# Optimization experiments

Hardware: AMD Instinct MI355X
Metric: run time of the kernel (lower is better)

## Reference

```python
import jax, jax.numpy as jnp
import numpy as np

VOXEL_SIZE = np.array([0.32, 0.32, 6.0], dtype=np.float32)
SPATIAL_SIZE = np.array([-74.88, 74.88, -74.88, 74.88, -3.0, 3.0], dtype=np.float32)
# voxel_spatial_size = ceil((max-min)/voxel_size) per dim -> [468, 468, 1]
GRID = np.array([int(np.ceil((SPATIAL_SIZE[2*i+1]-SPATIAL_SIZE[2*i])/VOXEL_SIZE[i])) for i in range(3)], dtype=np.int32)
# voxel origin = floor(min / voxel_size) -> [-234, -234, -1]
ORIGIN = np.floor(SPATIAL_SIZE[0::2] / VOXEL_SIZE).astype(np.int32)
VOL = int(np.prod(GRID))  # 468*468*1
# row-major id multipliers: prods[1:]+[1] -> [468, 1, 1]
SHIFT = np.array([int(np.prod(GRID[1:])), int(np.prod(GRID[2:])), 1], dtype=np.int32)
VOXEL_FEATURE_MIN = -1000.0

B, N, D_IN, MLP = 4, 100000, 16, 128


def setup_inputs() -> dict:
    key = jax.random.key(0)
    k1, k2, k3, k4, k5 = jax.random.split(key, 5)
    xy = jax.random.uniform(k1, (B, N, 2), minval=-80.0, maxval=80.0)
    z = jax.random.uniform(k2, (B, N, 1), minval=-4.0, maxval=4.0)
    point_xyz = jnp.concatenate([xy, z], axis=-1)
    point_feature = jax.random.normal(k3, (B, N, D_IN), dtype=jnp.float32)
    point_mask = jax.random.uniform(k4, (B, N)) < 0.95
    W = jax.random.normal(k5, (D_IN + 3, MLP), dtype=jnp.float32) * 0.1
    b = jnp.zeros((MLP,), dtype=jnp.float32)
    return {"point_xyz": point_xyz, "point_feature": point_feature,
            "point_mask": point_mask, "W": W, "b": b}


def reference(point_xyz, point_feature, point_mask, W, b):
    vs = jnp.asarray(VOXEL_SIZE, dtype=point_xyz.dtype)
    # PointToVoxel
    pvx_f = jnp.floor(point_xyz / vs)                      # [B,N,3] float voxel coords
    point_voxel_feature = point_xyz - pvx_f * vs           # delta within voxel
    pvx = pvx_f.astype(jnp.int32) - jnp.asarray(ORIGIN)    # shifted int voxel coords
    grid = jnp.asarray(GRID)
    in_bounds = jnp.all((pvx >= 0) & (pvx < grid), axis=-1)
    voxel_mask = in_bounds & point_mask                    # [B,N]
    vid = jnp.sum(pvx * jnp.asarray(SHIFT), axis=-1)       # [B,N]
    vid = vid + jnp.arange(B, dtype=jnp.int32)[:, None] * VOL
    vid = vid * voxel_mask.astype(jnp.int32)               # invalid -> 0
    # point net (Dense + ReLU) on [point_feature, voxel delta]
    feat = jnp.concatenate([point_feature, point_voxel_feature], axis=-1)
    mf = voxel_mask.astype(feat.dtype)[..., None]
    feat = feat * mf
    feat = jax.nn.relu(jnp.einsum('bnd,dk->bnk', feat, W) + b)
    feat = feat * mf
    # scatter-max into dense voxel grid
    seg = jax.ops.segment_max(feat.reshape(-1, MLP), vid.reshape(-1),
                              num_segments=B * VOL)
    seg = jnp.where(seg > VOXEL_FEATURE_MIN, seg, 0.0)
    # z dim is 1 -> squeezed: [B, 468, 468, MLP]
    return seg.reshape(B, int(GRID[0]), int(GRID[1]), MLP)
```

## Files before the change

kernel.cpp:

```cpp
#include <hip/hip_runtime.h>
#include <hip/hip_bf16.h>
#include <stdint.h>

#define BB   4
#define NN   100000
#define DIN  16
#define DF   19
#define KO   128
#define GX   468
#define GY   468
#define VOL  (GX * GY)
#define TOTAL (BB * NN)

__global__ __launch_bounds__(256) void zero_fill(float4* __restrict__ out, int n4) {
    int i = blockIdx.x * 256 + threadIdx.x;
    const int stride = gridDim.x * 256;
    const float4 z = make_float4(0.f, 0.f, 0.f, 0.f);
    for (; i < n4; i += stride) out[i] = z;
}

__global__ void detect_mask_kind(const uint4* __restrict__ mask_words,
                                 int* __restrict__ flag) {
    __shared__ int sA, sB;
    if (threadIdx.x == 0) { sA = 0; sB = 0; }
    __syncthreads();
    int a = 0, b = 0;
    #pragma unroll
    for (int it = 0; it < 4; ++it) {
        uint4 w = mask_words[it * 256 + threadIdx.x];
        unsigned lo = (w.x & 0xFFu) | (w.y & 0xFFu) | (w.z & 0xFFu) | (w.w & 0xFFu);
        unsigned hi = (w.x & 0xFFFFFF00u) | (w.y & 0xFFFFFF00u) |
                      (w.z & 0xFFFFFF00u) | (w.w & 0xFFFFFF00u);
        if (hi) a = 1;
        if (lo) b = 1;
    }
    if (a) atomicOr(&sA, 1);
    if (b) atomicOr(&sB, 1);
    __syncthreads();
    if (threadIdx.x == 0) flag[0] = (sA && sB) ? 1 : 4;
}

__global__ __launch_bounds__(256) void voxelize_kernel(
    const float* __restrict__ xyz,
    const float* __restrict__ pfeat,
    const unsigned char* __restrict__ mask_raw,
    const float* __restrict__ W,
    const float* __restrict__ bias,
    const int*   __restrict__ flag,
    float* __restrict__ out)
{
    __shared__ float sW[DF * KO];
    __shared__ float sb[KO];
    for (int i = threadIdx.x; i < DF * KO; i += 256) sW[i] = W[i];
    if (threadIdx.x < KO) sb[threadIdx.x] = bias[threadIdx.x];
    __syncthreads();

    const int elem4 = (flag[0] == 4);
    const int lane  = threadIdx.x & 63;
    const int wave  = blockIdx.x * 4 + (threadIdx.x >> 6);
    const int nwaves = gridDim.x * 4;
    const int chunk = (TOTAL + nwaves - 1) / nwaves;
    const int p0 = wave * chunk;
    const int p1 = min(p0 + chunk, TOTAL);

    const float b0 = sb[lane];
    const float b1 = sb[lane + 64];

    for (int p = p0; p < p1; ++p) {
        const float x = xyz[p * 3 + 0];
        const float y = xyz[p * 3 + 1];
        const float z = xyz[p * 3 + 2];
        bool m;
        if (elem4) m = (((const int*)mask_raw)[p] != 0);
        else       m = (mask_raw[p] != 0);
        const float fx = floorf(x / 0.32f);
        const float fy = floorf(y / 0.32f);
        const float fz = floorf(z / 6.0f);
        const int ix = (int)fx + 234;
        const int iy = (int)fy + 234;
        const int iz = (int)fz + 1;
        const bool inb = ((unsigned)ix < (unsigned)GX) &
                         ((unsigned)iy < (unsigned)GY) &
                         (iz == 0) & m;
        if (!inb) continue;

        float f[DF];
        const float4* pf4 = (const float4*)(pfeat + (size_t)p * DIN);
        float4 v0 = pf4[0], v1 = pf4[1], v2 = pf4[2], v3 = pf4[3];
        f[0]=v0.x; f[1]=v0.y; f[2]=v0.z; f[3]=v0.w;
        f[4]=v1.x; f[5]=v1.y; f[6]=v1.z; f[7]=v1.w;
        f[8]=v2.x; f[9]=v2.y; f[10]=v2.z; f[11]=v2.w;
        f[12]=v3.x; f[13]=v3.y; f[14]=v3.z; f[15]=v3.w;
        f[16] = x - fx * 0.32f;
        f[17] = y - fy * 0.32f;
        f[18] = z - fz * 6.0f;

        float acc0 = b0, acc1 = b1;
        #pragma unroll
        for (int d = 0; d < DF; ++d) {
            acc0 = fmaf(f[d], sW[d * KO + lane], acc0);
            acc1 = fmaf(f[d], sW[d * KO + 64 + lane], acc1);
        }
        acc0 = fmaxf(acc0, 0.0f);
        acc1 = fmaxf(acc1, 0.0f);

        const int bidx = p / NN;
        float* dst = out + (size_t)(bidx * VOL + ix * GY + iy) * KO;
        if (acc0 > 0.0f)
            atomicMax((int*)(dst + lane), __float_as_int(acc0));
        if (acc1 > 0.0f)
            atomicMax((int*)(dst + lane + 64), __float_as_int(acc1));
    }
}

extern "C" void kernel_launch(void* const* d_in, const int* in_sizes, int n_in,
                              void* d_out, int out_size, void* d_ws, size_t ws_size,
                              hipStream_t stream) {
    const float* xyz   = (const float*)d_in[0];
    const float* pfeat = (const float*)d_in[1];
    const unsigned char* mask = (const unsigned char*)d_in[2];
    const float* W     = (const float*)d_in[3];
    const float* bias  = (const float*)d_in[4];
    float* out = (float*)d_out;
    int*   flag = (int*)d_ws;

    const int n4 = out_size / 4;
    zero_fill<<<4096, 256, 0, stream>>>((float4*)out, n4);
    detect_mask_kind<<<1, 256, 0, stream>>>((const uint4*)mask, flag);
    voxelize_kernel<<<2048, 256, 0, stream>>>(xyz, pfeat, mask, W, bias, flag, out);
}
```

Baseline: 595.6 us.

## Replace atomic scatter-max with counting sort and per-voxel gather reduction

Points are bucketed by voxel using a count pass, a three-level prefix scan and a scatter into a sorted point list. One wave per voxel then recomputes the dense layer for its points, takes the max in registers and writes the output once, which folds in the separate zero-fill pass. This removes the global float atomicMax traffic and the full-output zero fill, in exchange for several extra small kernels and workspace buffers. Empty voxels are handled by the same kernel that writes the output.

```diff
diff --git a/kernel.cpp b/kernel.cpp
--- a/kernel.cpp
+++ b/kernel.cpp
@@ -4,20 +4,23 @@
 
 #define BB   4
 #define NN   100000
+#define TOTAL (BB * NN)
 #define DIN  16
 #define DF   19
 #define KO   128
 #define GX   468
 #define GY   468
 #define VOL  (GX * GY)
-#define TOTAL (BB * NN)
-
-__global__ __launch_bounds__(256) void zero_fill(float4* __restrict__ out, int n4) {
-    int i = blockIdx.x * 256 + threadIdx.x;
-    const int stride = gridDim.x * 256;
-    const float4 z = make_float4(0.f, 0.f, 0.f, 0.f);
-    for (; i < n4; i += stride) out[i] = z;
-}
+#define NV   (BB * VOL)
+#define NBLK ((NV + 1023) / 1024)
+
+#define WS_COUNTS   0
+#define WS_OFFSETS  (NV)
+#define WS_BSUM     (2 * NV)
+#define WS_PVID     (2 * NV + 1024)
+#define WS_PRANK    (2 * NV + 1024 + TOTAL)
+#define WS_PLIST    (2 * NV + 1024 + 2 * TOTAL)
+#define WS_FLAG     (2 * NV + 1024 + 3 * TOTAL)
 
 __global__ void detect_mask_kind(const uint4* __restrict__ mask_words,
                                  int* __restrict__ flag) {
@@ -40,50 +43,143 @@
     if (threadIdx.x == 0) flag[0] = (sA && sB) ? 1 : 4;
 }
 
-__global__ __launch_bounds__(256) void voxelize_kernel(
+__global__ __launch_bounds__(256) void zero_counts(int4* __restrict__ counts4) {
+    int i = blockIdx.x * 256 + threadIdx.x;
+    if (i < NV / 4) counts4[i] = make_int4(0, 0, 0, 0);
+}
+
+__global__ __launch_bounds__(256) void pass1_count(
+    const float* __restrict__ xyz,
+    const unsigned char* __restrict__ mask_raw,
+    const int* __restrict__ flag,
+    int* __restrict__ counts,
+    int* __restrict__ pvid,
+    int* __restrict__ prank)
+{
+    const int p = blockIdx.x * 256 + threadIdx.x;
+    if (p >= TOTAL) return;
+    const float x = xyz[p * 3 + 0];
+    const float y = xyz[p * 3 + 1];
+    const float z = xyz[p * 3 + 2];
+    bool m;
+    if (flag[0] == 4) m = (((const int*)mask_raw)[p] != 0);
+    else              m = (mask_raw[p] != 0);
+    const int ix = (int)floorf(x / 0.32f) + 234;
+    const int iy = (int)floorf(y / 0.32f) + 234;
+    const int iz = (int)floorf(z / 6.0f) + 1;
+    const bool inb = ((unsigned)ix < (unsigned)GX) &
+                     ((unsigned)iy < (unsigned)GY) &
+                     (iz == 0) & m;
+    int vid = -1;
+    if (inb) {
+        vid = (p / NN) * VOL + ix * GY + iy;
+        prank[p] = atomicAdd(&counts[vid], 1);
+    }
+    pvid[p] = vid;
+}
+
+__global__ __launch_bounds__(256) void scan_bsum(const int* __restrict__ counts,
+                                                 int* __restrict__ bsum) {
+    __shared__ int sdata[256];
+    const int t = threadIdx.x;
+    const int base = blockIdx.x * 1024 + t * 4;
+    int s = 0;
+    #pragma unroll
+    for (int j = 0; j < 4; ++j) {
+        const int i = base + j;
+        if (i < NV) s += counts[i];
+    }
+    sdata[t] = s;
+    __syncthreads();
+    for (int off = 128; off > 0; off >>= 1) {
+        if (t < off) sdata[t] += sdata[t + off];
+        __syncthreads();
+    }
+    if (t == 0) bsum[blockIdx.x] = sdata[0];
+}
+
+__global__ __launch_bounds__(1024) void scan_top(int* __restrict__ bsum) {
+    __shared__ int s[1024];
+    const int t = threadIdx.x;
+    const int v = (t < NBLK) ? bsum[t] : 0;
+    s[t] = v;
+    __syncthreads();
+    for (int off = 1; off < 1024; off <<= 1) {
+        const int tmp = (t >= off) ? s[t - off] : 0;
+        __syncthreads();
+        s[t] += tmp;
+        __syncthreads();
+    }
+    if (t < NBLK) bsum[t] = s[t] - v;
+}
+
+__global__ __launch_bounds__(256) void scan_offsets(const int* __restrict__ counts,
+                                                    const int* __restrict__ bsum,
+                                                    int* __restrict__ offsets) {
+    __shared__ int sdata[256];
+    const int t = threadIdx.x;
+    const int i0 = blockIdx.x * 1024 + t * 4;
+    int c[4];
+    #pragma unroll
+    for (int j = 0; j < 4; ++j)
+        c[j] = (i0 + j < NV) ? counts[i0 + j] : 0;
+    const int tsum = c[0] + c[1] + c[2] + c[3];
+    sdata[t] = tsum;
+    __syncthreads();
+    for (int off = 1; off < 256; off <<= 1) {
+        const int tmp = (t >= off) ? sdata[t - off] : 0;
+        __syncthreads();
+        sdata[t] += tmp;
+        __syncthreads();
+    }
+    int excl = sdata[t] - tsum + bsum[blockIdx.x];
+    #pragma unroll
+    for (int j = 0; j < 4; ++j) {
+        if (i0 + j < NV) { offsets[i0 + j] = excl; excl += c[j]; }
+    }
+}
+
+__global__ __launch_bounds__(256) void pass2_scatter(
+    const int* __restrict__ pvid,
+    const int* __restrict__ prank,
+    const int* __restrict__ offsets,
+    int* __restrict__ plist)
+{
+    const int p = blockIdx.x * 256 + threadIdx.x;
+    if (p >= TOTAL) return;
+    const int v = pvid[p];
+    if (v >= 0) plist[offsets[v] + prank[p]] = p;
+}
+
+__global__ __launch_bounds__(256) void pass3_write(
     const float* __restrict__ xyz,
     const float* __restrict__ pfeat,
-    const unsigned char* __restrict__ mask_raw,
     const float* __restrict__ W,
     const float* __restrict__ bias,
-    const int*   __restrict__ flag,
+    const int* __restrict__ counts,
+    const int* __restrict__ offsets,
+    const int* __restrict__ plist,
     float* __restrict__ out)
 {
-    __shared__ float sW[DF * KO];
-    __shared__ float sb[KO];
-    for (int i = threadIdx.x; i < DF * KO; i += 256) sW[i] = W[i];
-    if (threadIdx.x < KO) sb[threadIdx.x] = bias[threadIdx.x];
-    __syncthreads();
-
-    const int elem4 = (flag[0] == 4);
-    const int lane  = threadIdx.x & 63;
-    const int wave  = blockIdx.x * 4 + (threadIdx.x >> 6);
-    const int nwaves = gridDim.x * 4;
-    const int chunk = (TOTAL + nwaves - 1) / nwaves;
-    const int p0 = wave * chunk;
-    const int p1 = min(p0 + chunk, TOTAL);
-
-    const float b0 = sb[lane];
-    const float b1 = sb[lane + 64];
-
-    for (int p = p0; p < p1; ++p) {
+    const int lane = threadIdx.x & 63;
+    const int v = blockIdx.x * 4 + (threadIdx.x >> 6);
+    const int c = counts[v];
+    float2* dst = (float2*)(out + (size_t)v * KO) + lane;
+    if (c == 0) { *dst = make_float2(0.f, 0.f); return; }
+
+    const int o = offsets[v];
+    const float2* W2 = (const float2*)W;
+    float2 w[DF];
+    #pragma unroll
+    for (int d = 0; d < DF; ++d) w[d] = W2[d * 64 + lane];
+    const float2 bb = ((const float2*)bias)[lane];
+
+    float m0 = -3.0e38f, m1 = -3.0e38f;
+    for (int j = 0; j < c; ++j) {
+        const int p = plist[o + j];
         const float x = xyz[p * 3 + 0];
         const float y = xyz[p * 3 + 1];
         const float z = xyz[p * 3 + 2];
-        bool m;
-        if (elem4) m = (((const int*)mask_raw)[p] != 0);
-        else       m = (mask_raw[p] != 0);
-        const float fx = floorf(x / 0.32f);
-        const float fy = floorf(y / 0.32f);
-        const float fz = floorf(z / 6.0f);
-        const int ix = (int)fx + 234;
-        const int iy = (int)fy + 234;
-        const int iz = (int)fz + 1;
-        const bool inb = ((unsigned)ix < (unsigned)GX) &
-                         ((unsigned)iy < (unsigned)GY) &
-                         (iz == 0) & m;
-        if (!inb) continue;
-
         float f[DF];
         const float4* pf4 = (const float4*)(pfeat + (size_t)p * DIN);
         float4 v0 = pf4[0], v1 = pf4[1], v2 = pf4[2], v3 = pf4[3];
@@ -91,26 +187,20 @@
         f[4]=v1.x; f[5]=v1.y; f[6]=v1.z; f[7]=v1.w;
         f[8]=v2.x; f[9]=v2.y; f[10]=v2.z; f[11]=v2.w;
         f[12]=v3.x; f[13]=v3.y; f[14]=v3.z; f[15]=v3.w;
-        f[16] = x - fx * 0.32f;
-        f[17] = y - fy * 0.32f;
-        f[18] = z - fz * 6.0f;
-
-        float acc0 = b0, acc1 = b1;
+        f[16] = x - floorf(x / 0.32f) * 0.32f;
+        f[17] = y - floorf(y / 0.32f) * 0.32f;
+        f[18] = z - floorf(z / 6.0f) * 6.0f;
+
+        float a0 = bb.x, a1 = bb.y;
         #pragma unroll
         for (int d = 0; d < DF; ++d) {
-            acc0 = fmaf(f[d], sW[d * KO + lane], acc0);
-            acc1 = fmaf(f[d], sW[d * KO + 64 + lane], acc1);
+            a0 = fmaf(f[d], w[d].x, a0);
+            a1 = fmaf(f[d], w[d].y, a1);
         }
-        acc0 = fmaxf(acc0, 0.0f);
-        acc1 = fmaxf(acc1, 0.0f);
-
-        const int bidx = p / NN;
-        float* dst = out + (size_t)(bidx * VOL + ix * GY + iy) * KO;
-        if (acc0 > 0.0f)
-            atomicMax((int*)(dst + lane), __float_as_int(acc0));
-        if (acc1 > 0.0f)
-            atomicMax((int*)(dst + lane + 64), __float_as_int(acc1));
-    }
+        m0 = fmaxf(m0, a0);
+        m1 = fmaxf(m1, a1);
+    }
+    *dst = make_float2(fmaxf(m0, 0.f), fmaxf(m1, 0.f));
 }
 
 extern "C" void kernel_launch(void* const* d_in, const int* in_sizes, int n_in,
@@ -122,10 +212,25 @@
     const float* W     = (const float*)d_in[3];
     const float* bias  = (const float*)d_in[4];
     float* out = (float*)d_out;
-    int*   flag = (int*)d_ws;
-
-    const int n4 = out_size / 4;
-    zero_fill<<<4096, 256, 0, stream>>>((float4*)out, n4);
+    int* ws = (int*)d_ws;
+
+    int* counts  = ws + WS_COUNTS;
+    int* offsets = ws + WS_OFFSETS;
+    int* bsum    = ws + WS_BSUM;
+    int* pvid    = ws + WS_PVID;
+    int* prank   = ws + WS_PRANK;
+    int* plist   = ws + WS_PLIST;
+    int* flag    = ws + WS_FLAG;
+
     detect_mask_kind<<<1, 256, 0, stream>>>((const uint4*)mask, flag);
-    voxelize_kernel<<<2048, 256, 0, stream>>>(xyz, pfeat, mask, W, bias, flag, out);
-}
+    zero_counts<<<(NV / 4 + 255) / 256, 256, 0, stream>>>((int4*)counts);
+    pass1_count<<<(TOTAL + 255) / 256, 256, 0, stream>>>(xyz, mask, flag,
+                                                         counts, pvid, prank);
+    scan_bsum<<<NBLK, 256, 0, stream>>>(counts, bsum);
+    scan_top<<<1, 1024, 0, stream>>>(bsum);
+    scan_offsets<<<NBLK, 256, 0, stream>>>(counts, bsum, offsets);
+    pass2_scatter<<<(TOTAL + 255) / 256, 256, 0, stream>>>(pvid, prank,
+                                                           offsets, plist);
+    pass3_write<<<NV / 4, 256, 0, stream>>>(xyz, pfeat, W, bias,
+                                            counts, offsets, plist, out);
+}
```

Measured after the change: 654.5 us. +9.9%, slower.

## Bin points per voxel, then gather and reduce max without atomics

Applied to the files above, without the earlier changes.

Replaces the per-point scatter with float atomicMax by a two-pass scheme. The first pass bins point indices into fixed-capacity per-voxel lists using atomic counters. The second pass walks every voxel, recomputes the MLP for its points, takes the max in registers and writes the voxel row with plain stores. It also merges zero-fill and mask detection into one prep kernel. The costs are extra workspace (counts plus a CAP=16 list per voxel), a zeroing pass over the counts, redundant zero-filling of output that gather_write mostly overwrites, and silent truncation if a voxel ever holds more than 16 points.

```diff
diff --git a/kernel.cpp b/kernel.cpp
--- a/kernel.cpp
+++ b/kernel.cpp
@@ -4,112 +4,136 @@
 
 #define BB   4
 #define NN   100000
+#define TOTAL (BB * NN)
 #define DIN  16
 #define DF   19
 #define KO   128
 #define GX   468
 #define GY   468
 #define VOL  (GX * GY)
-#define TOTAL (BB * NN)
+#define NV   (BB * VOL)
+#define CAP  16
 
-__global__ __launch_bounds__(256) void zero_fill(float4* __restrict__ out, int n4) {
-    int i = blockIdx.x * 256 + threadIdx.x;
+#define WS_COUNTS   0
+#define WS_PLIST    (NV)
+#define WS_FLAG     (NV + NV * CAP)
+
+__global__ __launch_bounds__(256) void prep(
+    float4* __restrict__ out4,
+    int4*   __restrict__ counts4,
+    const uint4* __restrict__ mask_words,
+    int* __restrict__ flag)
+{
+    if (blockIdx.x == 0) {
+        __shared__ int sA, sB;
+        if (threadIdx.x == 0) { sA = 0; sB = 0; }
+        __syncthreads();
+        int a = 0, b = 0;
+        #pragma unroll
+        for (int it = 0; it < 4; ++it) {
+            uint4 w = mask_words[it * 256 + threadIdx.x];
+            unsigned lo = (w.x & 0xFFu) | (w.y & 0xFFu) | (w.z & 0xFFu) | (w.w & 0xFFu);
+            unsigned hi = (w.x & 0xFFFFFF00u) | (w.y & 0xFFFFFF00u) |
+                          (w.z & 0xFFFFFF00u) | (w.w & 0xFFFFFF00u);
+            if (hi) a = 1;
+            if (lo) b = 1;
+        }
+        if (a) atomicOr(&sA, 1);
+        if (b) atomicOr(&sB, 1);
+        __syncthreads();
+        if (threadIdx.x == 0) flag[0] = (sA && sB) ? 1 : 4;
+    }
+
     const int stride = gridDim.x * 256;
-    const float4 z = make_float4(0.f, 0.f, 0.f, 0.f);
-    for (; i < n4; i += stride) out[i] = z;
+    const int gid = blockIdx.x * 256 + threadIdx.x;
+    const float4 zf = make_float4(0.f, 0.f, 0.f, 0.f);
+    for (int i = gid; i < NV * (KO / 4); i += stride) out4[i] = zf;
+    const int4 zi = make_int4(0, 0, 0, 0);
+    for (int i = gid; i < NV / 4; i += stride) counts4[i] = zi;
 }
 
-__global__ void detect_mask_kind(const uint4* __restrict__ mask_words,
-                                 int* __restrict__ flag) {
-    __shared__ int sA, sB;
-    if (threadIdx.x == 0) { sA = 0; sB = 0; }
-    __syncthreads();
-    int a = 0, b = 0;
-    #pragma unroll
-    for (int it = 0; it < 4; ++it) {
-        uint4 w = mask_words[it * 256 + threadIdx.x];
-        unsigned lo = (w.x & 0xFFu) | (w.y & 0xFFu) | (w.z & 0xFFu) | (w.w & 0xFFu);
-        unsigned hi = (w.x & 0xFFFFFF00u) | (w.y & 0xFFFFFF00u) |
-                      (w.z & 0xFFFFFF00u) | (w.w & 0xFFFFFF00u);
-        if (hi) a = 1;
-        if (lo) b = 1;
+__global__ __launch_bounds__(256) void pass1_bin(
+    const float* __restrict__ xyz,
+    const unsigned char* __restrict__ mask_raw,
+    const int* __restrict__ flag,
+    int* __restrict__ counts,
+    int* __restrict__ plist)
+{
+    const int p = blockIdx.x * 256 + threadIdx.x;
+    if (p >= TOTAL) return;
+    const float x = xyz[p * 3 + 0];
+    const float y = xyz[p * 3 + 1];
+    const float z = xyz[p * 3 + 2];
+    bool m;
+    if (flag[0] == 4) m = (((const int*)mask_raw)[p] != 0);
+    else              m = (mask_raw[p] != 0);
+    const int ix = (int)floorf(x / 0.32f) + 234;
+    const int iy = (int)floorf(y / 0.32f) + 234;
+    const int iz = (int)floorf(z / 6.0f) + 1;
+    const bool inb = ((unsigned)ix < (unsigned)GX) &
+                     ((unsigned)iy < (unsigned)GY) &
+                     (iz == 0) & m;
+    if (inb) {
+        const int vid = (p / NN) * VOL + ix * GY + iy;
+        const int rank = atomicAdd(&counts[vid], 1);
+        if (rank < CAP) plist[vid * CAP + rank] = p;
     }
-    if (a) atomicOr(&sA, 1);
-    if (b) atomicOr(&sB, 1);
-    __syncthreads();
-    if (threadIdx.x == 0) flag[0] = (sA && sB) ? 1 : 4;
 }
 
-__global__ __launch_bounds__(256) void voxelize_kernel(
+__global__ __launch_bounds__(256) void gather_write(
     const float* __restrict__ xyz,
     const float* __restrict__ pfeat,
-    const unsigned char* __restrict__ mask_raw,
     const float* __restrict__ W,
     const float* __restrict__ bias,
-    const int*   __restrict__ flag,
+    const int* __restrict__ counts,
+    const int* __restrict__ plist,
     float* __restrict__ out)
 {
-    __shared__ float sW[DF * KO];
-    __shared__ float sb[KO];
-    for (int i = threadIdx.x; i < DF * KO; i += 256) sW[i] = W[i];
-    if (threadIdx.x < KO) sb[threadIdx.x] = bias[threadIdx.x];
-    __syncthreads();
+    const int lane = threadIdx.x & 63;
+    const int wave = (blockIdx.x * 256 + threadIdx.x) >> 6;
+    const int v0 = wave * 8;
 
-    const int elem4 = (flag[0] == 4);
-    const int lane  = threadIdx.x & 63;
-    const int wave  = blockIdx.x * 4 + (threadIdx.x >> 6);
-    const int nwaves = gridDim.x * 4;
-    const int chunk = (TOTAL + nwaves - 1) / nwaves;
-    const int p0 = wave * chunk;
-    const int p1 = min(p0 + chunk, TOTAL);
+    const float2* W2 = (const float2*)W;
+    float2 w[DF];
+    #pragma unroll
+    for (int d = 0; d < DF; ++d) w[d] = W2[d * 64 + lane];
+    const float2 bb = ((const float2*)bias)[lane];
 
-    const float b0 = sb[lane];
-    const float b1 = sb[lane + 64];
+    for (int j = 0; j < 8; ++j) {
+        const int v = v0 + j;
+        int c = counts[v];
+        if (c == 0) continue;
+        c = min(c, CAP);
+        const int o = v * CAP;
 
-    for (int p = p0; p < p1; ++p) {
-        const float x = xyz[p * 3 + 0];
-        const float y = xyz[p * 3 + 1];
-        const float z = xyz[p * 3 + 2];
-        bool m;
-        if (elem4) m = (((const int*)mask_raw)[p] != 0);
-        else       m = (mask_raw[p] != 0);
-        const float fx = floorf(x / 0.32f);
-        const float fy = floorf(y / 0.32f);
-        const float fz = floorf(z / 6.0f);
-        const int ix = (int)fx + 234;
-        const int iy = (int)fy + 234;
-        const int iz = (int)fz + 1;
-        const bool inb = ((unsigned)ix < (unsigned)GX) &
-                         ((unsigned)iy < (unsigned)GY) &
-                         (iz == 0) & m;
-        if (!inb) continue;
+        float m0 = -3.0e38f, m1 = -3.0e38f;
+        for (int t = 0; t < c; ++t) {
+            const int p = plist[o + t];
+            const float x = xyz[p * 3 + 0];
+            const float y = xyz[p * 3 + 1];
+            const float z = xyz[p * 3 + 2];
+            float f[DF];
+            const float4* pf4 = (const float4*)(pfeat + (size_t)p * DIN);
+            float4 v0f = pf4[0], v1f = pf4[1], v2f = pf4[2], v3f = pf4[3];
+            f[0]=v0f.x; f[1]=v0f.y; f[2]=v0f.z; f[3]=v0f.w;
+            f[4]=v1f.x; f[5]=v1f.y; f[6]=v1f.z; f[7]=v1f.w;
+            f[8]=v2f.x; f[9]=v2f.y; f[10]=v2f.z; f[11]=v2f.w;
+            f[12]=v3f.x; f[13]=v3f.y; f[14]=v3f.z; f[15]=v3f.w;
+            f[16] = x - floorf(x / 0.32f) * 0.32f;
+            f[17] = y - floorf(y / 0.32f) * 0.32f;
+            f[18] = z - floorf(z / 6.0f) * 6.0f;
 
-        float f[DF];
-        const float4* pf4 = (const float4*)(pfeat + (size_t)p * DIN);
-        float4 v0 = pf4[0], v1 = pf4[1], v2 = pf4[2], v3 = pf4[3];
-        f[0]=v0.x; f[1]=v0.y; f[2]=v0.z; f[3]=v0.w;
-        f[4]=v1.x; f[5]=v1.y; f[6]=v1.z; f[7]=v1.w;
-        f[8]=v2.x; f[9]=v2.y; f[10]=v2.z; f[11]=v2.w;
-        f[12]=v3.x; f[13]=v3.y; f[14]=v3.z; f[15]=v3.w;
-        f[16] = x - fx * 0.32f;
-        f[17] = y - fy * 0.32f;
-        f[18] = z - fz * 6.0f;
-
-        float acc0 = b0, acc1 = b1;
-        #pragma unroll
-        for (int d = 0; d < DF; ++d) {
-            acc0 = fmaf(f[d], sW[d * KO + lane], acc0);
-            acc1 = fmaf(f[d], sW[d * KO + 64 + lane], acc1);
+            float a0 = bb.x, a1 = bb.y;
+            #pragma unroll
+            for (int d = 0; d < DF; ++d) {
+                a0 = fmaf(f[d], w[d].x, a0);
+                a1 = fmaf(f[d], w[d].y, a1);
+            }
+            m0 = fmaxf(m0, a0);
+            m1 = fmaxf(m1, a1);
         }
-        acc0 = fmaxf(acc0, 0.0f);
-        acc1 = fmaxf(acc1, 0.0f);
-
-        const int bidx = p / NN;
-        float* dst = out + (size_t)(bidx * VOL + ix * GY + iy) * KO;
-        if (acc0 > 0.0f)
-            atomicMax((int*)(dst + lane), __float_as_int(acc0));
-        if (acc1 > 0.0f)
-            atomicMax((int*)(dst + lane + 64), __float_as_int(acc1));
+        float2* dst = (float2*)(out + (size_t)v * KO) + lane;
+        *dst = make_float2(fmaxf(m0, 0.f), fmaxf(m1, 0.f));
     }
 }
 
@@ -122,10 +146,16 @@
     const float* W     = (const float*)d_in[3];
     const float* bias  = (const float*)d_in[4];
     float* out = (float*)d_out;
-    int*   flag = (int*)d_ws;
+    int* ws = (int*)d_ws;
 
-    const int n4 = out_size / 4;
-    zero_fill<<<4096, 256, 0, stream>>>((float4*)out, n4);
-    detect_mask_kind<<<1, 256, 0, stream>>>((const uint4*)mask, flag);
-    voxelize_kernel<<<2048, 256, 0, stream>>>(xyz, pfeat, mask, W, bias, flag, out);
+    int* counts = ws + WS_COUNTS;
+    int* plist  = ws + WS_PLIST;
+    int* flag   = ws + WS_FLAG;
+
+    prep<<<4096, 256, 0, stream>>>((float4*)out, (int4*)counts,
+                                   (const uint4*)mask, flag);
+    pass1_bin<<<(TOTAL + 255) / 256, 256, 0, stream>>>(xyz, mask, flag,
+                                                       counts, plist);
+    gather_write<<<NV / 32, 256, 0, stream>>>(xyz, pfeat, W, bias,
+                                              counts, plist, out);
 }
```

New measurement: 644.4 us. +8.2%, slower.
